# Optimization experiments

Measured on AMD Instinct MI355X. Metric: run time of the kernel, lower is better.

## Reference

```python
import jax, jax.numpy as jnp
import numpy as np

N_NODES = 100000
N_EDGES = 3200000
H, D = 3, 12  # heads, per-head dim; H*D == node_hidden_dim == 36
NEG_SLOPE = 0.2


def setup_inputs() -> dict:
    key = jax.random.key(0)
    ks = jax.random.split(key, 11)
    s = 0.1
    return {
        "node_features": jax.random.normal(ks[0], (N_NODES, 36), jnp.float32),
        "src": jax.random.randint(ks[1], (N_EDGES,), 0, N_NODES),
        "dst": jax.random.randint(ks[2], (N_EDGES,), 0, N_NODES),
        "lin0_w": jax.random.normal(ks[3], (36, 36), jnp.float32) * s,
        "lin0_b": jax.random.normal(ks[4], (36,), jnp.float32) * s,
        "fc_w": jax.random.normal(ks[5], (3, 36, 36), jnp.float32) * s,
        "attn_l": jax.random.normal(ks[6], (3, H, D), jnp.float32) * s,
        "attn_r": jax.random.normal(ks[7], (3, H, D), jnp.float32) * s,
        "gat_bias": jax.random.normal(ks[8], (3, 36), jnp.float32) * s,
        "out_w": jax.random.normal(ks[9], (36, 36), jnp.float32) * s,
        "out_b": jax.random.normal(ks[10], (36,), jnp.float32) * s,
    }


def _gat_layer(h, src, dst, fc_w, a_l, a_r, bias):
    n = h.shape[0]
    feat = (h @ fc_w).reshape(n, H, D)                      # (N,H,D)
    el = jnp.sum(feat * a_l, axis=-1)                       # (N,H)
    er = jnp.sum(feat * a_r, axis=-1)                       # (N,H)
    e = el[src] + er[dst]                                   # (E,H)
    e = jnp.where(e >= 0, e, NEG_SLOPE * e)                 # leaky_relu(0.2)
    # edge softmax over incoming edges of each dst node (numerically stable)
    m = jax.ops.segment_max(e, dst, num_segments=n)         # (N,H)
    m = jnp.where(jnp.isfinite(m), m, 0.0)                  # zero-degree guard
    ee = jnp.exp(e - m[dst])                                # (E,H)
    denom = jax.ops.segment_sum(ee, dst, num_segments=n)    # (N,H)
    alpha = ee / jnp.maximum(denom[dst], 1e-9)              # (E,H)
    msg = feat[src] * alpha[:, :, None]                     # (E,H,D)
    rst = jax.ops.segment_sum(msg, dst, num_segments=n)     # (N,H,D)
    # residual (Identity since in_feats == H*D) + bias, then ELU
    rst = rst + h.reshape(n, H, D) + bias.reshape(1, H, D)
    return jax.nn.elu(rst).reshape(n, H * D)


def reference(node_features, src, dst, lin0_w, lin0_b, fc_w, attn_l, attn_r, gat_bias, out_w, out_b):
    h = node_features @ lin0_w + lin0_b
    for l in range(3):
        h = _gat_layer(h, src, dst, fc_w[l], attn_l[l], attn_r[l], gat_bias[l])
    return h @ out_w + out_b
```

## Files before the change

kernel.cpp:

```cpp
#include <hip/hip_runtime.h>
#include <math.h>

#define HID 36
#define NH 3
#define HD 12
#define BSHIFT 13
#define NBUCK 13
#define PSHIFT 8
#define PCHUNK 8192
#define CSRCAP 4096

typedef _Float16 f16;
typedef unsigned short u16;


__global__ void hist2_kernel(const int* __restrict__ dst, int* __restrict__ M,
                             int E, int C, int np) {
    __shared__ int h[512];
    int t = threadIdx.x;
    int c = blockIdx.x;
    for (int i = t; i < 512; i += blockDim.x) h[i] = 0;
    __syncthreads();
    int i0 = c * PCHUNK;
    int i1 = min(i0 + PCHUNK, E);
    for (int i = i0 + t; i < i1; i += blockDim.x)
        atomicAdd(&h[dst[i] >> PSHIFT], 1);
    __syncthreads();
    for (int b = t; b < np; b += blockDim.x)
        M[(size_t)b * C + c] = h[b];
}

__global__ void base_scan_kernel(const int* __restrict__ M, int* __restrict__ BaseT,
                                 int* __restrict__ T, int C, int np) {
    __shared__ int tmp[512];
    int b = blockIdx.x;
    int t = threadIdx.x;
    int v = (t < C) ? M[(size_t)b * C + t] : 0;
    tmp[t] = v;
    __syncthreads();
    for (int ofs = 1; ofs < 512; ofs <<= 1) {
        int x = 0;
        if (t >= ofs) x = tmp[t - ofs];
        __syncthreads();
        tmp[t] += x;
        __syncthreads();
    }
    if (t < C) BaseT[(size_t)t * 512 + b] = tmp[t] - v;
    if (t == 511) T[b] = tmp[511];
}

__global__ void scan_small_kernel(const int* __restrict__ T, int* __restrict__ poff, int np) {
    __shared__ int tmp[512];
    int t = threadIdx.x;
    int v = (t < np) ? T[t] : 0;
    tmp[t] = v;
    __syncthreads();
    for (int ofs = 1; ofs < 512; ofs <<= 1) {
        int x = 0;
        if (t >= ofs) x = tmp[t - ofs];
        __syncthreads();
        tmp[t] += x;
        __syncthreads();
    }
    int excl = tmp[t] - v;
    if (t < np) poff[t] = excl;
    if (t == np - 1) poff[np] = excl + v;
}

__global__ void part_scatter_kernel(const int* __restrict__ src, const int* __restrict__ dst,
                                    const int* __restrict__ BaseT, const int* __restrict__ poff,
                                    int* __restrict__ part, int E, int np) {
    __shared__ int h[512];
    __shared__ int base[512];
    int t = threadIdx.x;
    int c = blockIdx.x;
    for (int i = t; i < 512; i += blockDim.x) h[i] = 0;
    for (int b = t; b < np; b += blockDim.x)
        base[b] = poff[b] + BaseT[(size_t)c * 512 + b];
    __syncthreads();
    int i0 = c * PCHUNK;
    int i1 = min(i0 + PCHUNK, E);
    for (int i = i0 + t; i < i1; i += blockDim.x) {
        int d = dst[i];
        int bin = d >> PSHIFT;
        int r = atomicAdd(&h[bin], 1);
        part[base[bin] + r] = (src[i] << PSHIFT) | (d & ((1 << PSHIFT) - 1));
    }
}

__global__ void bucket_csr_kernel(const int* __restrict__ part, const int* __restrict__ T,
                                  const int* __restrict__ poff,
                                  int* __restrict__ csr, int* __restrict__ off,
                                  u16* __restrict__ counts, int n, int E) {
    __shared__ int cnt[256 * NBUCK];
    __shared__ int psum[256];
    int p = blockIdx.x;
    int t = threadIdx.x;
    int dbase = p << PSHIFT;
    int nd = min(256, n - dbase);
    int nc = nd * NBUCK;
    for (int i = t; i < nc; i += blockDim.x) cnt[i] = 0;
    __syncthreads();
    int cnt_p = T[p];
    int e0 = poff[p];
    const int* pp = part + e0;
    for (int i = t; i < cnt_p; i += blockDim.x) {
        int e = pp[i];
        atomicAdd(&cnt[(e & 255) * NBUCK + ((e >> PSHIFT) >> BSHIFT)], 1);
    }
    __syncthreads();
    int sum = 0;
    if (t < nd) {
        for (int k = 0; k < NBUCK; ++k) {
            int c = cnt[t * NBUCK + k];
            cnt[t * NBUCK + k] = sum;
            sum += c;
        }
    }
    psum[t] = (t < nd) ? sum : 0;
    __syncthreads();
    for (int ofs = 1; ofs < 256; ofs <<= 1) {
        int x = 0;
        if (t >= ofs) x = psum[t - ofs];
        __syncthreads();
        psum[t] += x;
        __syncthreads();
    }
    int dexcl = (t > 0) ? psum[t - 1] : 0;
    int start = e0 + dexcl;
    if (t < nd) {
        for (int k = 0; k < NBUCK; ++k) cnt[t * NBUCK + k] += start;
        off[dbase + t] = start;
    }
    __syncthreads();
    for (int i = t; i < cnt_p; i += blockDim.x) {
        int e = pp[i];
        int s = e >> PSHIFT;
        int idx = (e & 255) * NBUCK + (s >> BSHIFT);
        int pos = atomicAdd(&cnt[idx], 1);
        csr[pos] = s * 48;
    }
    __syncthreads();
    if (t < nd) {
        union { u16 cc[16]; uint4 q[2]; } u;
        int prev = start;
        for (int k = 0; k < NBUCK; ++k) {
            int end = cnt[t * NBUCK + k];
            u.cc[k] = (u16)(end - prev);
            prev = end;
        }
        u.cc[13] = 0; u.cc[14] = 0; u.cc[15] = 0;
        uint4* cp = (uint4*)(counts + (size_t)(dbase + t) * 16);
        cp[0] = u.q[0];
        cp[1] = u.q[1];
    }
    if (p == 0 && t == 0) off[n] = E;
}


__device__ __forceinline__ void edge_accum(uint4 qa, uint4 qb, float ern,
                                           float& denom, float* acc) {
    union { uint4 q[2]; f16 hx[16]; } v;
    v.q[0] = qa;
    v.q[1] = qb;
    float e = (float)v.hx[12] + ern;
    e = (e >= 0.f) ? e : 0.2f * e;
    float w = __expf(e);
    denom += w;
#pragma unroll
    for (int k = 0; k < HD; ++k) acc[k] += w * (float)v.hx[k];
}

__global__ void lin0tr_kernel(const float* __restrict__ x, const float* __restrict__ w0,
                              const float* __restrict__ b0, const float* __restrict__ fcw,
                              const float* __restrict__ al, const float* __restrict__ ar,
                              float* __restrict__ h, f16* __restrict__ packed,
                              float* __restrict__ er, int n) {
    __shared__ float W0[HID * HID];
    __shared__ float W1[HID * HID];
    __shared__ float Bs[HID], ALs[HID], ARs[HID];
    int t = threadIdx.x;
    for (int i = t; i < HID * HID; i += 256) { W0[i] = w0[i]; W1[i] = fcw[i]; }
    if (t < HID) { Bs[t] = b0[t]; ALs[t] = al[t]; ARs[t] = ar[t]; }
    __syncthreads();
    int node = blockIdx.x * 256 + t;
    if (node >= n) return;
    const float4* xp = (const float4*)(x + (size_t)node * HID);
    float h0[HID];
#pragma unroll
    for (int j = 0; j < HID; ++j) h0[j] = Bs[j];
#pragma unroll
    for (int kk = 0; kk < HID / 4; ++kk) {
        float4 xv = xp[kk];
        const float* w = &W0[(4 * kk) * HID];
#pragma unroll
        for (int j = 0; j < HID; ++j)
            h0[j] += xv.x * w[j] + xv.y * w[HID + j] + xv.z * w[2 * HID + j] + xv.w * w[3 * HID + j];
    }
    float* hp = h + (size_t)node * HID;
#pragma unroll
    for (int j = 0; j < HID; ++j) hp[j] = h0[j];
    float feat[HID];
#pragma unroll
    for (int j = 0; j < HID; ++j) feat[j] = 0.f;
#pragma unroll
    for (int k = 0; k < HID; ++k) {
        float hv = h0[k];
        const float* w = &W1[k * HID];
#pragma unroll
        for (int j = 0; j < HID; ++j) feat[j] += hv * w[j];
    }
    union { f16 hx[48]; uint4 q[6]; } u;
#pragma unroll
    for (int hh = 0; hh < NH; ++hh) {
        float sl = 0.f, sr = 0.f;
#pragma unroll
        for (int d = 0; d < HD; ++d) {
            sl += feat[hh * HD + d] * ALs[hh * HD + d];
            sr += feat[hh * HD + d] * ARs[hh * HD + d];
        }
#pragma unroll
        for (int d = 0; d < HD; ++d) u.hx[hh * 16 + d] = (f16)feat[hh * HD + d];
        u.hx[hh * 16 + 12] = (f16)sl;
        u.hx[hh * 16 + 13] = (f16)0.f;
        u.hx[hh * 16 + 14] = (f16)0.f;
        u.hx[hh * 16 + 15] = (f16)0.f;
        er[node * NH + hh] = sr;
    }
    uint4* prow = (uint4*)(packed + (size_t)node * 48);
#pragma unroll
    for (int q = 0; q < 6; ++q) prow[q] = u.q[q];
}

__global__ void __launch_bounds__(192)
aggtr_kernel(const f16* __restrict__ packed_in, const float* __restrict__ er_in,
             const float* __restrict__ hcur, const u16* __restrict__ counts,
             const int* __restrict__ off, const int* __restrict__ csr,
             const float* __restrict__ bias, const float* __restrict__ wnext,
             const float* __restrict__ aln, const float* __restrict__ arn,
             float* __restrict__ hnext, f16* __restrict__ packed_out,
             float* __restrict__ er_out, int n) {
    __shared__ float Wsh[HID * HID];
    __shared__ float ALs[HID], ARs[HID];
    __shared__ int smbuf[CSRCAP];
    int t = threadIdx.x;
    for (int i = t; i < HID * HID; i += 192) Wsh[i] = wnext[i];
    if (t < HID) { ALs[t] = aln[t]; ARs[t] = arn[t]; }
    int ln = t / 3, hh = t - ln * 3;
    int nb0 = blockIdx.x * 64;
    int node = nb0 + ln;
    bool active = (node < n);

    int e0 = off[nb0];
    int e1 = off[min(nb0 + 64, n)];
    int span = e1 - e0;
    for (int i = t; i < span && i < CSRCAP; i += 192) smbuf[i] = csr[e0 + i];

    int j = 0;
    float ern = 0.f;
    union { u16 cc[16]; uint4 q[2]; } u;
    u.q[0] = make_uint4(0, 0, 0, 0);
    u.q[1] = make_uint4(0, 0, 0, 0);
    if (active) {
        j = off[node] - e0;
        ern = er_in[node * NH + hh];
        const uint4* cp = (const uint4*)(counts + (size_t)node * 16);
        u.q[0] = cp[0];
        u.q[1] = cp[1];
    }
    const f16* pb = packed_in + hh * 16;
    __syncthreads();

    float denom = 0.f;
    float acc[HD];
#pragma unroll
    for (int k = 0; k < HD; ++k) acc[k] = 0.f;

    for (int kb = 0; kb < NBUCK; ++kb) {
        int c = u.cc[kb];
        for (; c >= 2; c -= 2, j += 2) {
            int o0 = (j < CSRCAP) ? smbuf[j] : csr[e0 + j];
            int o1 = (j + 1 < CSRCAP) ? smbuf[j + 1] : csr[e0 + j + 1];
            const uint4* r0 = (const uint4*)(pb + o0);
            const uint4* r1 = (const uint4*)(pb + o1);
            uint4 a0 = r0[0], b0 = r0[1];
            uint4 a1 = r1[0], b1 = r1[1];
            edge_accum(a0, b0, ern, denom, acc);
            edge_accum(a1, b1, ern, denom, acc);
        }
        if (c) {
            int o = (j < CSRCAP) ? smbuf[j] : csr[e0 + j];
            ++j;
            const uint4* r = (const uint4*)(pb + o);
            edge_accum(r[0], r[1], ern, denom, acc);
        }
        __syncthreads();
    }

    float* hsh = (float*)smbuf;
    float v[HD];
#pragma unroll
    for (int k = 0; k < HD; ++k) v[k] = 0.f;
    if (active) {
        float inv = 1.f / fmaxf(denom, 1e-9f);
        int base = node * HID + hh * HD;
        const float4* hc = (const float4*)(hcur + base);
        float4 h0 = hc[0], h1 = hc[1], h2 = hc[2];
        float hres[HD] = {h0.x, h0.y, h0.z, h0.w, h1.x, h1.y, h1.z, h1.w, h2.x, h2.y, h2.z, h2.w};
#pragma unroll
        for (int k = 0; k < HD; ++k) {
            float x = acc[k] * inv + hres[k] + bias[hh * HD + k];
            v[k] = (x > 0.f) ? x : expm1f(x);
        }
        float4* hp = (float4*)(hnext + base);
        hp[0] = make_float4(v[0], v[1], v[2], v[3]);
        hp[1] = make_float4(v[4], v[5], v[6], v[7]);
        hp[2] = make_float4(v[8], v[9], v[10], v[11]);
    }
#pragma unroll
    for (int k = 0; k < HD; ++k) hsh[ln * 37 + hh * HD + k] = v[k];
    __syncthreads();

    float feat[HD];
#pragma unroll
    for (int d = 0; d < HD; ++d) feat[d] = 0.f;
    const float* hrow = &hsh[ln * 37];
#pragma unroll 4
    for (int k = 0; k < HID; ++k) {
        float hv = hrow[k];
        const float* w = &Wsh[k * HID + hh * HD];
#pragma unroll
        for (int d = 0; d < HD; ++d) feat[d] += hv * w[d];
    }
    if (!active) return;
    float sl = 0.f, sr = 0.f;
#pragma unroll
    for (int d = 0; d < HD; ++d) {
        sl += feat[d] * ALs[hh * HD + d];
        sr += feat[d] * ARs[hh * HD + d];
    }
    union { f16 hx[16]; uint4 q[2]; } o;
#pragma unroll
    for (int d = 0; d < HD; ++d) o.hx[d] = (f16)feat[d];
    o.hx[12] = (f16)sl;
    o.hx[13] = (f16)0.f; o.hx[14] = (f16)0.f; o.hx[15] = (f16)0.f;
    uint4* prow = (uint4*)(packed_out + (size_t)node * 48 + hh * 16);
    prow[0] = o.q[0];
    prow[1] = o.q[1];
    er_out[node * NH + hh] = sr;
}

__global__ void __launch_bounds__(192)
aggout_kernel(const f16* __restrict__ packed_in, const float* __restrict__ er_in,
              const float* __restrict__ hcur, const u16* __restrict__ counts,
              const int* __restrict__ off, const int* __restrict__ csr,
              const float* __restrict__ bias, const float* __restrict__ ow,
              const float* __restrict__ ob, float* __restrict__ out, int n) {
    __shared__ float Wsh[HID * HID];
    __shared__ float OBs[HID];
    __shared__ int smbuf[CSRCAP];
    int t = threadIdx.x;
    for (int i = t; i < HID * HID; i += 192) Wsh[i] = ow[i];
    if (t < HID) OBs[t] = ob[t];
    int ln = t / 3, hh = t - ln * 3;
    int nb0 = blockIdx.x * 64;
    int node = nb0 + ln;
    bool active = (node < n);

    int e0 = off[nb0];
    int e1 = off[min(nb0 + 64, n)];
    int span = e1 - e0;
    for (int i = t; i < span && i < CSRCAP; i += 192) smbuf[i] = csr[e0 + i];

    int j = 0;
    float ern = 0.f;
    union { u16 cc[16]; uint4 q[2]; } u;
    u.q[0] = make_uint4(0, 0, 0, 0);
    u.q[1] = make_uint4(0, 0, 0, 0);
    if (active) {
        j = off[node] - e0;
        ern = er_in[node * NH + hh];
        const uint4* cp = (const uint4*)(counts + (size_t)node * 16);
        u.q[0] = cp[0];
        u.q[1] = cp[1];
    }
    const f16* pb = packed_in + hh * 16;
    __syncthreads();

    float denom = 0.f;
    float acc[HD];
#pragma unroll
    for (int k = 0; k < HD; ++k) acc[k] = 0.f;

    for (int kb = 0; kb < NBUCK; ++kb) {
        int c = u.cc[kb];
        for (; c >= 2; c -= 2, j += 2) {
            int o0 = (j < CSRCAP) ? smbuf[j] : csr[e0 + j];
            int o1 = (j + 1 < CSRCAP) ? smbuf[j + 1] : csr[e0 + j + 1];
            const uint4* r0 = (const uint4*)(pb + o0);
            const uint4* r1 = (const uint4*)(pb + o1);
            uint4 a0 = r0[0], b0 = r0[1];
            uint4 a1 = r1[0], b1 = r1[1];
            edge_accum(a0, b0, ern, denom, acc);
            edge_accum(a1, b1, ern, denom, acc);
        }
        if (c) {
            int o = (j < CSRCAP) ? smbuf[j] : csr[e0 + j];
            ++j;
            const uint4* r = (const uint4*)(pb + o);
            edge_accum(r[0], r[1], ern, denom, acc);
        }
        __syncthreads();
    }

    float* hsh = (float*)smbuf;
    float v[HD];
#pragma unroll
    for (int k = 0; k < HD; ++k) v[k] = 0.f;
    if (active) {
        float inv = 1.f / fmaxf(denom, 1e-9f);
        int base = node * HID + hh * HD;
        const float4* hc = (const float4*)(hcur + base);
        float4 h0 = hc[0], h1 = hc[1], h2 = hc[2];
        float hres[HD] = {h0.x, h0.y, h0.z, h0.w, h1.x, h1.y, h1.z, h1.w, h2.x, h2.y, h2.z, h2.w};
#pragma unroll
        for (int k = 0; k < HD; ++k) {
            float x = acc[k] * inv + hres[k] + bias[hh * HD + k];
            v[k] = (x > 0.f) ? x : expm1f(x);
        }
    }
#pragma unroll
    for (int k = 0; k < HD; ++k) hsh[ln * 37 + hh * HD + k] = v[k];
    __syncthreads();

    float feat[HD];
#pragma unroll
    for (int d = 0; d < HD; ++d) feat[d] = OBs[hh * HD + d];
    const float* hrow = &hsh[ln * 37];
#pragma unroll 4
    for (int k = 0; k < HID; ++k) {
        float hv = hrow[k];
        const float* w = &Wsh[k * HID + hh * HD];
#pragma unroll
        for (int d = 0; d < HD; ++d) feat[d] += hv * w[d];
    }
    if (!active) return;
    float4* op = (float4*)(out + (size_t)node * HID + hh * HD);
    op[0] = make_float4(feat[0], feat[1], feat[2], feat[3]);
    op[1] = make_float4(feat[4], feat[5], feat[6], feat[7]);
    op[2] = make_float4(feat[8], feat[9], feat[10], feat[11]);
}


extern "C" void kernel_launch(void* const* d_in, const int* in_sizes, int n_in,
                              void* d_out, int out_size, void* d_ws, size_t ws_size,
                              hipStream_t stream) {
    const float* xnf = (const float*)d_in[0];
    const int* src = (const int*)d_in[1];
    const int* dst = (const int*)d_in[2];
    const float* l0w = (const float*)d_in[3];
    const float* l0b = (const float*)d_in[4];
    const float* fcw = (const float*)d_in[5];
    const float* al  = (const float*)d_in[6];
    const float* ar  = (const float*)d_in[7];
    const float* gb  = (const float*)d_in[8];
    const float* ow  = (const float*)d_in[9];
    const float* ob  = (const float*)d_in[10];
    float* out = (float*)d_out;
    const int N = in_sizes[0] / HID;
    const int E = in_sizes[1];
    const int NP = (N + (1 << PSHIFT) - 1) >> PSHIFT;
    const int C = (E + PCHUNK - 1) / PCHUNK;

    char* p = (char*)d_ws;
    auto alloc = [&](size_t bytes) {
        char* r = p;
        p += (bytes + 255) & ~(size_t)255;
        return r;
    };
    int* part    = (int*)alloc((size_t)E * 4);
    int* M       = (int*)alloc((size_t)NP * C * 4);
    int* BaseT   = (int*)alloc((size_t)C * 512 * 4);
    int* T       = (int*)alloc((size_t)NP * 4);
    int* poff    = (int*)alloc((size_t)(NP + 1) * 4);
    int* off     = (int*)alloc((size_t)(N + 1) * 4);
    int* csr     = (int*)alloc((size_t)E * 4);
    u16* counts  = (u16*)alloc((size_t)N * 16 * 2);
    float* ha    = (float*)alloc((size_t)N * HID * 4);
    float* hb    = (float*)alloc((size_t)N * HID * 4);
    f16* pkA     = (f16*)alloc((size_t)N * 48 * 2);
    f16* pkB     = (f16*)alloc((size_t)N * 48 * 2);
    float* erA   = (float*)alloc((size_t)N * NH * 4);
    float* erB   = (float*)alloc((size_t)N * NH * 4);

    hist2_kernel<<<C, 256, 0, stream>>>(dst, M, E, C, NP);
    base_scan_kernel<<<NP, 512, 0, stream>>>(M, BaseT, T, C, NP);
    scan_small_kernel<<<1, 512, 0, stream>>>(T, poff, NP);
    part_scatter_kernel<<<C, 256, 0, stream>>>(src, dst, BaseT, poff, part, E, NP);
    bucket_csr_kernel<<<NP, 256, 0, stream>>>(part, T, poff, csr, off, counts, N, E);

    int nblk = (N + 255) / 256;
    int fblk = (N + 63) / 64;

    lin0tr_kernel<<<nblk, 256, 0, stream>>>(xnf, l0w, l0b, fcw, al, ar, ha, pkA, erA, N);

    aggtr_kernel<<<fblk, 192, 0, stream>>>(pkA, erA, ha, counts, off, csr, gb,
                                           fcw + (size_t)1 * HID * HID, al + HID, ar + HID,
                                           hb, pkB, erB, N);
    aggtr_kernel<<<fblk, 192, 0, stream>>>(pkB, erB, hb, counts, off, csr, gb + HID,
                                           fcw + (size_t)2 * HID * HID, al + 2 * HID, ar + 2 * HID,
                                           ha, pkA, erA, N);
    aggout_kernel<<<fblk, 192, 0, stream>>>(pkA, erA, ha, counts, off, csr, gb + 2 * HID,
                                            ow, ob, out, N);
}
```

Baseline: 402.9 us.

## Drop per-bucket barriers and counts, sweep contiguous edge range with 4-way unroll

The aggregation kernels previously walked edges bucket by bucket (sorted by source range) with a block-wide barrier after each of 13 buckets, which kept the threads of a block reading similar source regions of the packed features. The new code drops the per-node bucket counts array and those barriers. Each thread now sweeps its contiguous CSR range using off[node+1], unrolled by four, with a templated path that takes indices from shared memory when the block's edges fit and from global memory otherwise. This removes the barrier stalls and the counts traffic, but gives up the synchronized locality of the gathers across the block, which may raise cache misses.

Measured after the change: 388.8 us. 1.04x faster.

```diff
diff --git a/kernel.cpp b/kernel.cpp
--- a/kernel.cpp
+++ b/kernel.cpp
@@ -11,7 +11,6 @@
 #define CSRCAP 4096
 
 typedef _Float16 f16;
-typedef unsigned short u16;
 
 
 __global__ void hist2_kernel(const int* __restrict__ dst, int* __restrict__ M,
@@ -91,7 +90,7 @@
 __global__ void bucket_csr_kernel(const int* __restrict__ part, const int* __restrict__ T,
                                   const int* __restrict__ poff,
                                   int* __restrict__ csr, int* __restrict__ off,
-                                  u16* __restrict__ counts, int n, int E) {
+                                  int n, int E) {
     __shared__ int cnt[256 * NBUCK];
     __shared__ int psum[256];
     int p = blockIdx.x;
@@ -139,20 +138,6 @@
         int idx = (e & 255) * NBUCK + (s >> BSHIFT);
         int pos = atomicAdd(&cnt[idx], 1);
         csr[pos] = s * 48;
-    }
-    __syncthreads();
-    if (t < nd) {
-        union { u16 cc[16]; uint4 q[2]; } u;
-        int prev = start;
-        for (int k = 0; k < NBUCK; ++k) {
-            int end = cnt[t * NBUCK + k];
-            u.cc[k] = (u16)(end - prev);
-            prev = end;
-        }
-        u.cc[13] = 0; u.cc[14] = 0; u.cc[15] = 0;
-        uint4* cp = (uint4*)(counts + (size_t)(dbase + t) * 16);
-        cp[0] = u.q[0];
-        cp[1] = u.q[1];
     }
     if (p == 0 && t == 0) off[n] = E;
 }
@@ -171,6 +156,37 @@
     for (int k = 0; k < HD; ++k) acc[k] += w * (float)v.hx[k];
 }
 
+template <bool FITS>
+__device__ __forceinline__ void sweep_edges(const int* __restrict__ smbuf,
+                                            const int* __restrict__ csre,
+                                            int j, int jend, const f16* __restrict__ pb,
+                                            float ern, float& denom, float* acc) {
+    int m = jend - j;
+    for (; m >= 4; m -= 4, j += 4) {
+        int o0 = FITS ? smbuf[j]     : csre[j];
+        int o1 = FITS ? smbuf[j + 1] : csre[j + 1];
+        int o2 = FITS ? smbuf[j + 2] : csre[j + 2];
+        int o3 = FITS ? smbuf[j + 3] : csre[j + 3];
+        const uint4* r0 = (const uint4*)(pb + o0);
+        const uint4* r1 = (const uint4*)(pb + o1);
+        const uint4* r2 = (const uint4*)(pb + o2);
+        const uint4* r3 = (const uint4*)(pb + o3);
+        uint4 a0 = r0[0], b0 = r0[1];
+        uint4 a1 = r1[0], b1 = r1[1];
+        uint4 a2 = r2[0], b2 = r2[1];
+        uint4 a3 = r3[0], b3 = r3[1];
+        edge_accum(a0, b0, ern, denom, acc);
+        edge_accum(a1, b1, ern, denom, acc);
+        edge_accum(a2, b2, ern, denom, acc);
+        edge_accum(a3, b3, ern, denom, acc);
+    }
+    for (; m > 0; --m, ++j) {
+        int o = FITS ? smbuf[j] : csre[j];
+        const uint4* r = (const uint4*)(pb + o);
+        edge_accum(r[0], r[1], ern, denom, acc);
+    }
+}
+
 __global__ void lin0tr_kernel(const float* __restrict__ x, const float* __restrict__ w0,
                               const float* __restrict__ b0, const float* __restrict__ fcw,
                               const float* __restrict__ al, const float* __restrict__ ar,
@@ -234,7 +250,7 @@
 
 __global__ void __launch_bounds__(192)
 aggtr_kernel(const f16* __restrict__ packed_in, const float* __restrict__ er_in,
-             const float* __restrict__ hcur, const u16* __restrict__ counts,
+             const float* __restrict__ hcur,
              const int* __restrict__ off, const int* __restrict__ csr,
              const float* __restrict__ bias, const float* __restrict__ wnext,
              const float* __restrict__ aln, const float* __restrict__ arn,
@@ -254,19 +270,16 @@
     int e0 = off[nb0];
     int e1 = off[min(nb0 + 64, n)];
     int span = e1 - e0;
-    for (int i = t; i < span && i < CSRCAP; i += 192) smbuf[i] = csr[e0 + i];
-
-    int j = 0;
+    bool fits = (span <= CSRCAP);
+    if (fits)
+        for (int i = t; i < span; i += 192) smbuf[i] = csr[e0 + i];
+
+    int j0 = 0, j1 = 0;
     float ern = 0.f;
-    union { u16 cc[16]; uint4 q[2]; } u;
-    u.q[0] = make_uint4(0, 0, 0, 0);
-    u.q[1] = make_uint4(0, 0, 0, 0);
     if (active) {
-        j = off[node] - e0;
+        j0 = off[node] - e0;
+        j1 = off[node + 1] - e0;
         ern = er_in[node * NH + hh];
-        const uint4* cp = (const uint4*)(counts + (size_t)node * 16);
-        u.q[0] = cp[0];
-        u.q[1] = cp[1];
     }
     const f16* pb = packed_in + hh * 16;
     __syncthreads();
@@ -276,26 +289,9 @@
 #pragma unroll
     for (int k = 0; k < HD; ++k) acc[k] = 0.f;
 
-    for (int kb = 0; kb < NBUCK; ++kb) {
-        int c = u.cc[kb];
-        for (; c >= 2; c -= 2, j += 2) {
-            int o0 = (j < CSRCAP) ? smbuf[j] : csr[e0 + j];
-            int o1 = (j + 1 < CSRCAP) ? smbuf[j + 1] : csr[e0 + j + 1];
-            const uint4* r0 = (const uint4*)(pb + o0);
-            const uint4* r1 = (const uint4*)(pb + o1);
-            uint4 a0 = r0[0], b0 = r0[1];
-            uint4 a1 = r1[0], b1 = r1[1];
-            edge_accum(a0, b0, ern, denom, acc);
-            edge_accum(a1, b1, ern, denom, acc);
-        }
-        if (c) {
-            int o = (j < CSRCAP) ? smbuf[j] : csr[e0 + j];
-            ++j;
-            const uint4* r = (const uint4*)(pb + o);
-            edge_accum(r[0], r[1], ern, denom, acc);
-        }
-        __syncthreads();
-    }
+    if (fits) sweep_edges<true>(smbuf, csr + e0, j0, j1, pb, ern, denom, acc);
+    else      sweep_edges<false>(smbuf, csr + e0, j0, j1, pb, ern, denom, acc);
+    __syncthreads();
 
     float* hsh = (float*)smbuf;
     float v[HD];
@@ -352,7 +348,7 @@
 
 __global__ void __launch_bounds__(192)
 aggout_kernel(const f16* __restrict__ packed_in, const float* __restrict__ er_in,
-              const float* __restrict__ hcur, const u16* __restrict__ counts,
+              const float* __restrict__ hcur,
               const int* __restrict__ off, const int* __restrict__ csr,
               const float* __restrict__ bias, const float* __restrict__ ow,
               const float* __restrict__ ob, float* __restrict__ out, int n) {
@@ -370,19 +366,16 @@
     int e0 = off[nb0];
     int e1 = off[min(nb0 + 64, n)];
     int span = e1 - e0;
-    for (int i = t; i < span && i < CSRCAP; i += 192) smbuf[i] = csr[e0 + i];
-
-    int j = 0;
+    bool fits = (span <= CSRCAP);
+    if (fits)
+        for (int i = t; i < span; i += 192) smbuf[i] = csr[e0 + i];
+
+    int j0 = 0, j1 = 0;
     float ern = 0.f;
-    union { u16 cc[16]; uint4 q[2]; } u;
-    u.q[0] = make_uint4(0, 0, 0, 0);
-    u.q[1] = make_uint4(0, 0, 0, 0);
     if (active) {
-        j = off[node] - e0;
+        j0 = off[node] - e0;
+        j1 = off[node + 1] - e0;
         ern = er_in[node * NH + hh];
-        const uint4* cp = (const uint4*)(counts + (size_t)node * 16);
-        u.q[0] = cp[0];
-        u.q[1] = cp[1];
     }
     const f16* pb = packed_in + hh * 16;
     __syncthreads();
@@ -392,26 +385,9 @@
 #pragma unroll
     for (int k = 0; k < HD; ++k) acc[k] = 0.f;
 
-    for (int kb = 0; kb < NBUCK; ++kb) {
-        int c = u.cc[kb];
-        for (; c >= 2; c -= 2, j += 2) {
-            int o0 = (j < CSRCAP) ? smbuf[j] : csr[e0 + j];
-            int o1 = (j + 1 < CSRCAP) ? smbuf[j + 1] : csr[e0 + j + 1];
-            const uint4* r0 = (const uint4*)(pb + o0);
-            const uint4* r1 = (const uint4*)(pb + o1);
-            uint4 a0 = r0[0], b0 = r0[1];
-            uint4 a1 = r1[0], b1 = r1[1];
-            edge_accum(a0, b0, ern, denom, acc);
-            edge_accum(a1, b1, ern, denom, acc);
-        }
-        if (c) {
-            int o = (j < CSRCAP) ? smbuf[j] : csr[e0 + j];
-            ++j;
-            const uint4* r = (const uint4*)(pb + o);
-            edge_accum(r[0], r[1], ern, denom, acc);
-        }
-        __syncthreads();
-    }
+    if (fits) sweep_edges<true>(smbuf, csr + e0, j0, j1, pb, ern, denom, acc);
+    else      sweep_edges<false>(smbuf, csr + e0, j0, j1, pb, ern, denom, acc);
+    __syncthreads();
 
     float* hsh = (float*)smbuf;
     float v[HD];
@@ -485,7 +461,6 @@
     int* poff    = (int*)alloc((size_t)(NP + 1) * 4);
     int* off     = (int*)alloc((size_t)(N + 1) * 4);
     int* csr     = (int*)alloc((size_t)E * 4);
-    u16* counts  = (u16*)alloc((size_t)N * 16 * 2);
     float* ha    = (float*)alloc((size_t)N * HID * 4);
     float* hb    = (float*)alloc((size_t)N * HID * 4);
     f16* pkA     = (f16*)alloc((size_t)N * 48 * 2);
@@ -497,19 +472,19 @@
     base_scan_kernel<<<NP, 512, 0, stream>>>(M, BaseT, T, C, NP);
     scan_small_kernel<<<1, 512, 0, stream>>>(T, poff, NP);
     part_scatter_kernel<<<C, 256, 0, stream>>>(src, dst, BaseT, poff, part, E, NP);
-    bucket_csr_kernel<<<NP, 256, 0, stream>>>(part, T, poff, csr, off, counts, N, E);
+    bucket_csr_kernel<<<NP, 256, 0, stream>>>(part, T, poff, csr, off, N, E);
 
     int nblk = (N + 255) / 256;
     int fblk = (N + 63) / 64;
 
     lin0tr_kernel<<<nblk, 256, 0, stream>>>(xnf, l0w, l0b, fcw, al, ar, ha, pkA, erA, N);
 
-    aggtr_kernel<<<fblk, 192, 0, stream>>>(pkA, erA, ha, counts, off, csr, gb,
+    aggtr_kernel<<<fblk, 192, 0, stream>>>(pkA, erA, ha, off, csr, gb,
                                            fcw + (size_t)1 * HID * HID, al + HID, ar + HID,
                                            hb, pkB, erB, N);
-    aggtr_kernel<<<fblk, 192, 0, stream>>>(pkB, erB, hb, counts, off, csr, gb + HID,
+    aggtr_kernel<<<fblk, 192, 0, stream>>>(pkB, erB, hb, off, csr, gb + HID,
                                            fcw + (size_t)2 * HID * HID, al + 2 * HID, ar + 2 * HID,
                                            ha, pkA, erA, N);
-    aggout_kernel<<<fblk, 192, 0, stream>>>(pkA, erA, ha, counts, off, csr, gb + 2 * HID,
+    aggout_kernel<<<fblk, 192, 0, stream>>>(pkA, erA, ha, off, csr, gb + 2 * HID,
                                             ow, ob, out, N);
 }
```
